# Optimization experiments

Hardware: AMD Instinct MI355X
Metric: run time of the kernel (lower is better)

## Reference

```python
import jax, jax.numpy as jnp
import numpy as np

NUM_HEADS = 4
IN_CHANNELS = 256
SCALE = IN_CHANNELS ** (-0.5)  # scaled=True uses in_channels, not hidden


def setup_inputs() -> dict:
    key = jax.random.key(0)
    ks = jax.random.split(key, 6)
    B, C, H, W = 8, 256, 48, 48
    hid = 128
    std_e = (2.0 / (3 * hid)) ** 0.5   # kaiming fan_out for 1x1 conv
    std_o = (2.0 / C) ** 0.5
    return {
        "x0": jax.random.normal(ks[0], (B, C, H, W), jnp.float32),
        "x1": jax.random.normal(ks[1], (B, C, H, W), jnp.float32),
        "embed_w0": jax.random.normal(ks[2], (3 * hid, C), jnp.float32) * std_e,
        "embed_b0": jnp.zeros((3 * hid,), jnp.float32),
        "embed_w1": jax.random.normal(ks[3], (3 * hid, C), jnp.float32) * std_e,
        "embed_b1": jnp.zeros((3 * hid,), jnp.float32),
        "out_w0": jax.random.normal(ks[4], (hid * NUM_HEADS, C), jnp.float32) * std_o,
        "out_b0": jnp.zeros((C,), jnp.float32),
        "out_w1": jax.random.normal(ks[5], (hid * NUM_HEADS, C), jnp.float32) * std_o,
        "out_b1": jnp.zeros((C,), jnp.float32),
    }


def _embed(x, w, b):
    # 1x1 conv: [B,C,H,W] x [3h,C] -> [B,3h,H,W], then flatten spatial and split q/k/v
    e = jnp.einsum('bchw,oc->bohw', x, w) + b[None, :, None, None]
    B, O, H, W = e.shape
    e = e.reshape(B, O, H * W)
    return jnp.split(e, 3, axis=1)  # each [B, h, N]


def _attend(q, k, v):
    # q from the OTHER stream; softmax over keys (last dim)
    attn = jax.nn.softmax(jnp.einsum('bcm,bcn->bmn', q, k) * SCALE, axis=-1)
    return jnp.einsum('bmn,bcn->bcm', attn, v)  # [B, h, N]


def _output(h, x, w, b):
    # all NUM_HEADS heads are identical (same embed conv reused per head),
    # so the concat along channels is a tile of one head.
    hh = jnp.tile(h, (1, NUM_HEADS, 1))  # [B, h*nh, N]
    # 1x1 transposed conv == pointwise linear with weight [h*nh, C]
    o = jnp.einsum('bcm,co->bom', hh, w) + b[None, :, None]
    return o.reshape(x.shape) + x  # residual


def reference(x0, x1, embed_w0, embed_b0, embed_w1, embed_b1,
              out_w0, out_b0, out_w1, out_b1):
    q0, k0, v0 = _embed(x0, embed_w0, embed_b0)
    q1, k1, v1 = _embed(x1, embed_w1, embed_b1)
    h0 = _attend(q1, k0, v0)  # stream 0 queried by stream 1's q
    h1 = _attend(q0, k1, v1)
    out0 = _output(h0, x0, out_w0, out_b0)
    out1 = _output(h1, x1, out_w1, out_b1)
    return (out0, out1)
```

## Files before the change

### kernel.cpp

```cpp
#include <hip/hip_runtime.h>
#include <stdint.h>

#define B_   8
#define C_   256
#define N_   2304
#define HID  128
#define O3   384
#define NH   4
#define SCALE 0.0625f
#define QPRE 0.09016844f

typedef unsigned short u16;
typedef short  bf8  __attribute__((ext_vector_type(8)));
typedef float  f4   __attribute__((ext_vector_type(4)));
typedef u16    u16x8 __attribute__((ext_vector_type(8)));
typedef u16    u16x4 __attribute__((ext_vector_type(4)));

#define MFMA(a,b,c) __builtin_amdgcn_mfma_f32_16x16x32_bf16((a),(b),(c),0,0,0)

static __device__ __forceinline__ u16 f2bf(float f){
    union { float f; unsigned int i; } v; v.f = f;
    unsigned int r = v.i + 0x7FFFu + ((v.i >> 16) & 1u);
    return (u16)(r >> 16);
}
static __device__ __forceinline__ float fexp2(float x){
#if __has_builtin(__builtin_amdgcn_exp2f)
    return __builtin_amdgcn_exp2f(x);
#else
    return __expf(x * 0.69314718f);
#endif
}
static __device__ __forceinline__ u16 hi16(float f){
    union { float f; unsigned int i; } v; v.f = f;
    return (u16)(v.i >> 16);
}
static __device__ __forceinline__ void dma16(const void* g, void* l){
    __builtin_amdgcn_global_load_lds(
        (const __attribute__((address_space(1))) void*)g,
        (__attribute__((address_space(3))) void*)l, 16, 0, 0);
}

__global__ __launch_bounds__(256, 4) void k_embed_fused(
        const float* __restrict__ x0, const float* __restrict__ x1,
        const float* __restrict__ ew0, const float* __restrict__ ew1,
        const float* __restrict__ ow0, const float* __restrict__ ow1,
        const float* __restrict__ b0, const float* __restrict__ b1,
        u16* __restrict__ Qc, u16* __restrict__ Kc, u16* __restrict__ Vc,
        u16* __restrict__ weff){
    __shared__ __align__(16) u16 tmp[256*36];
    __shared__ __align__(16) u16 Xs[32*280];
    int t = threadIdx.x;

    if (blockIdx.y == 16){
        int bx = blockIdx.x;
        if (bx >= 64) return;
        int gid = bx*256 + t;
        int s = gid >> 13, oc = (gid >> 5) & 255, hc0 = (gid & 31) * 4;
        const float* w = s ? ow1 : ow0;
        u16x4 v;
        #pragma unroll
        for (int i = 0; i < 4; ++i){
            float acc = 0.f;
            #pragma unroll
            for (int h = 0; h < NH; ++h) acc += w[(h*HID + hc0 + i)*C_ + oc];
            v[i] = f2bf(acc);
        }
        *reinterpret_cast<u16x4*>(&weff[(s*C_ + oc)*HID + hc0]) = v;
        return;
    }

    int z = blockIdx.y, bb = z >> 1, s = z & 1;
    const float* X    = (s ? x1 : x0) + (size_t)bb * (C_ * N_);
    const float* Wf32 = s ? ew1 : ew0;
    const float* bias = s ? b1 : b0;
    int n0 = blockIdx.x * 32;
    int lane = t & 63, wave = t >> 6;
    int l16 = lane & 15, quad = lane >> 4;

    {
        int cbase = t >> 3, cq = t & 7;
        float4 xr[8];
        #pragma unroll
        for (int rep = 0; rep < 8; ++rep)
            xr[rep] = *reinterpret_cast<const float4*>(
                &X[(size_t)(cbase + rep*32) * N_ + n0 + cq*4]);
        #pragma unroll
        for (int rep = 0; rep < 8; ++rep){
            int c = cbase + rep*32;
            u16x4 v;
            v[0] = f2bf(xr[rep].x); v[1] = f2bf(xr[rep].y);
            v[2] = f2bf(xr[rep].z); v[3] = f2bf(xr[rep].w);
            *reinterpret_cast<u16x4*>(&tmp[c*36 + cq*4]) = v;
        }
    }
    __syncthreads();
    {
        int n = t & 31, c8b = t >> 5;
        #pragma unroll
        for (int rep = 0; rep < 4; ++rep){
            int c8 = c8b + rep*8;
            u16x8 v;
            #pragma unroll
            for (int j = 0; j < 8; ++j) v[j] = tmp[(c8*8 + j)*36 + n];
            *reinterpret_cast<u16x8*>(&Xs[n*280 + c8*8]) = v;
        }
    }
    __syncthreads();

    size_t zq = (size_t)z * (N_ * HID);
    int ncw = blockIdx.x >> 1;
    u16* Es = tmp;
    for (int og = 0; og < 6; ++og){
        int o0 = og*64 + wave*16;
        f4 acc[2] = {f4{0,0,0,0}, f4{0,0,0,0}};
        #pragma unroll
        for (int kk = 0; kk < 8; ++kk){
            const float* wp = &Wf32[(size_t)(o0 + l16)*C_ + kk*32 + quad*8];
            float4 wa = *reinterpret_cast<const float4*>(wp);
            float4 wb = *reinterpret_cast<const float4*>(wp + 4);
            bf8 a;
            a[0] = (short)f2bf(wa.x); a[1] = (short)f2bf(wa.y);
            a[2] = (short)f2bf(wa.z); a[3] = (short)f2bf(wa.w);
            a[4] = (short)f2bf(wb.x); a[5] = (short)f2bf(wb.y);
            a[6] = (short)f2bf(wb.z); a[7] = (short)f2bf(wb.w);
            #pragma unroll
            for (int nt = 0; nt < 2; ++nt){
                bf8 bv = *reinterpret_cast<const bf8*>(
                    &Xs[(nt*16 + l16)*280 + kk*32 + quad*8]);
                acc[nt] = MFMA(a, bv, acc[nt]);
            }
        }
        float4 bv4 = *reinterpret_cast<const float4*>(&bias[o0 + quad*4]);
        float bb4[4] = {bv4.x, bv4.y, bv4.z, bv4.w};
        #pragma unroll
        for (int nt = 0; nt < 2; ++nt)
            #pragma unroll
            for (int r = 0; r < 4; ++r){
                float e = acc[nt][r] + bb4[r];
                if (og < 2) e *= QPRE;
                Es[(wave*16 + quad*4 + r)*40 + nt*16 + l16] = f2bf(e);
            }
        __syncthreads();
        if (og < 2){
            int n = t & 31, g8 = t >> 5;
            u16x8 v;
            #pragma unroll
            for (int j = 0; j < 8; ++j) v[j] = Es[(g8*8 + j)*40 + n];
            int ng = n0 + n;
            *reinterpret_cast<u16x8*>(&Qc[zq + (size_t)(ng>>4)*2048
                    + (og*8 + g8)*128 + (ng & 15)*8]) = v;
        } else if (og < 4){
            int n = t & 31, cc = t >> 5;
            u16x8 v;
            #pragma unroll
            for (int j = 0; j < 8; ++j) v[j] = Es[(cc*8 + j)*40 + n];
            *reinterpret_cast<u16x8*>(&Kc[zq + (size_t)(ncw*16 + (og-2)*8 + cc)*512
                    + ((n0 + n) & 63)*8]) = v;
        } else {
            int hl = t & 63, pp = t >> 6;
            u16x8 v = *reinterpret_cast<const u16x8*>(&Es[hl*40 + pp*8]);
            int p = ((n0 + pp*8) >> 3) & 7;
            *reinterpret_cast<u16x8*>(&Vc[zq + (size_t)(ncw*8 + p)*1024
                    + ((og-4)*64 + hl)*8]) = v;
        }
        __syncthreads();
    }
}

__global__ __launch_bounds__(256, 3) void k_attn_out(const u16* __restrict__ Qt,
        const u16* __restrict__ Kc, const u16* __restrict__ Vc,
        const u16* __restrict__ weff,
        const float* __restrict__ ob0, const float* __restrict__ ob1,
        const float* __restrict__ x0, const float* __restrict__ x1,
        float* __restrict__ out){
    __shared__ __align__(16) u16 kbuf[64*128];
    __shared__ __align__(16) u16 vbuf[64*128];
    __shared__ __align__(16) u16 smem[8*16*72];
    int bx = blockIdx.x;
    int xcd = bx & 7, t = bx >> 3;
    int z  = xcd*2 + (t >= 36 ? 1 : 0);
    int mt = (t >= 36) ? (t - 36) : t;
    int b = z >> 1, s = z & 1;
    const u16* Q = Qt + (size_t)(b*2 + (1 - s)) * (N_ * HID);
    const u16* K = Kc + (size_t)(b*2 + s)       * (N_ * HID);
    const u16* V = Vc + (size_t)(b*2 + s)       * (N_ * HID);
    const u16* Wf   = weff + (size_t)s * (C_ * HID);
    const float* bias = s ? ob1 : ob0;
    const float* X = (s ? x1 : x0) + (size_t)b * (C_ * N_);
    float* O = out + (size_t)s * ((size_t)B_ * C_ * N_) + (size_t)b * (C_ * N_);
    int lane = threadIdx.x & 63, wave = threadIdx.x >> 6;
    int l16 = lane & 15, quad = lane >> 4;
    int m0 = mt * 64 + wave * 16;

    bf8 aq[4];
    {
        const u16* Qb = Q + (size_t)(m0 >> 4)*2048 + l16*8;
        #pragma unroll
        for (int kk = 0; kk < 4; ++kk)
            aq[kk] = *reinterpret_cast<const bf8*>(&Qb[(kk*4 + quad)*128]);
    }

    bf8 ones;
    #pragma unroll
    for (int j = 0; j < 8; ++j) ones[j] = (short)0x3F80;

    f4 oacc[8];
    #pragma unroll
    for (int ct = 0; ct < 8; ++ct) oacc[ct] = f4{0,0,0,0};
    f4 sumacc = f4{0,0,0,0};

    const char* Kb = (const char*)K;
    const char* Vb = (const char*)V;

    for (int nc = 0; nc < N_/64; ++nc){
        __syncthreads();
        #pragma unroll
        for (int j = 0; j < 4; ++j){
            int ik = wave*4 + j;
            dma16(Kb + ((size_t)(nc*16 + ik)*512 + lane*8)*2, &kbuf[ik*512]);
        }
        #pragma unroll
        for (int j = 0; j < 4; ++j){
            int iv = wave*4 + j;
            dma16(Vb + ((size_t)(nc*8 + (iv>>1))*1024 + (iv&1)*512 + lane*8)*2,
                  &vbuf[iv*512]);
        }
        __syncthreads();
        f4 sacc[4] = {f4{0,0,0,0}, f4{0,0,0,0}, f4{0,0,0,0}, f4{0,0,0,0}};
        #pragma unroll
        for (int kk = 0; kk < 4; ++kk)
            #pragma unroll
            for (int nt = 0; nt < 4; ++nt){
                bf8 bk = *reinterpret_cast<const bf8*>(&kbuf[((kk*4+quad)*64 + nt*16 + l16)*8]);
                sacc[nt] = MFMA(aq[kk], bk, sacc[nt]);
            }
        u16* pw = smem + (wave*2 + (nc & 1)) * (16*72);
        #pragma unroll
        for (int nt = 0; nt < 4; ++nt)
            #pragma unroll
            for (int r = 0; r < 4; ++r)
                pw[(quad*4 + r)*72 + nt*16 + l16] = hi16(fexp2(sacc[nt][r]));
        #pragma unroll
        for (int kk2 = 0; kk2 < 2; ++kk2){
            bf8 ap = *reinterpret_cast<const bf8*>(&pw[l16*72 + kk2*32 + quad*8]);
            sumacc = MFMA(ap, ones, sumacc);
            #pragma unroll
            for (int ct = 0; ct < 8; ++ct){
                bf8 bv = *reinterpret_cast<const bf8*>(&vbuf[((kk2*4+quad)*128 + ct*16 + l16)*8]);
                oacc[ct] = MFMA(ap, bv, oacc[ct]);
            }
        }
    }

    __syncthreads();
    float inv[4];
    #pragma unroll
    for (int r = 0; r < 4; ++r) inv[r] = 1.0f / sumacc[r];
    #pragma unroll
    for (int ct = 0; ct < 8; ++ct)
        #pragma unroll
        for (int r = 0; r < 4; ++r)
            smem[(wave*16 + quad*4 + r)*136 + ct*16 + l16] = f2bf(oacc[ct][r] * inv[r]);
    __syncthreads();

    int mb = mt * 64;
    int oc0 = wave * 64;
    f4 acc2[4][4];
    #pragma unroll
    for (int ot = 0; ot < 4; ++ot)
        #pragma unroll
        for (int nt = 0; nt < 4; ++nt) acc2[ot][nt] = f4{0,0,0,0};
    #pragma unroll
    for (int kk = 0; kk < 4; ++kk){
        bf8 bh[4];
        #pragma unroll
        for (int nt = 0; nt < 4; ++nt)
            bh[nt] = *reinterpret_cast<const bf8*>(&smem[(nt*16 + l16)*136 + kk*32 + quad*8]);
        #pragma unroll
        for (int ot = 0; ot < 4; ++ot){
            bf8 a = *reinterpret_cast<const bf8*>(&Wf[(oc0 + ot*16 + l16)*HID + kk*32 + quad*8]);
            #pragma unroll
            for (int nt = 0; nt < 4; ++nt)
                acc2[ot][nt] = MFMA(a, bh[nt], acc2[ot][nt]);
        }
    }
    #pragma unroll
    for (int ot = 0; ot < 4; ++ot)
        #pragma unroll
        for (int nt = 0; nt < 4; ++nt){
            int m = mb + nt*16 + l16;
            #pragma unroll
            for (int r = 0; r < 4; ++r){
                int oc = oc0 + ot*16 + quad*4 + r;
                O[(size_t)oc*N_ + m] = acc2[ot][nt][r] + bias[oc] + X[(size_t)oc*N_ + m];
            }
        }
}

extern "C" void kernel_launch(void* const* d_in, const int* in_sizes, int n_in,
                              void* d_out, int out_size, void* d_ws, size_t ws_size,
                              hipStream_t stream){
    const float* x0  = (const float*)d_in[0];
    const float* x1  = (const float*)d_in[1];
    const float* ew0 = (const float*)d_in[2];
    const float* eb0 = (const float*)d_in[3];
    const float* ew1 = (const float*)d_in[4];
    const float* eb1 = (const float*)d_in[5];
    const float* ow0 = (const float*)d_in[6];
    const float* ob0 = (const float*)d_in[7];
    const float* ow1 = (const float*)d_in[8];
    const float* ob1 = (const float*)d_in[9];

    u16* ws = (u16*)d_ws;
    const size_t QT_E = (size_t)16 * N_ * HID;
    u16* Qc   = ws;
    u16* Kc   = Qc + QT_E;
    u16* Vc   = Kc + QT_E;
    u16* weff = Vc + QT_E;

    k_embed_fused<<<dim3(72, 17), dim3(256), 0, stream>>>(
        x0, x1, ew0, ew1, ow0, ow1, eb0, eb1, Qc, Kc, Vc, weff);
    k_attn_out   <<<dim3(576),    dim3(256), 0, stream>>>(
        Qc, Kc, Vc, weff, ob0, ob1, x0, x1, (float*)d_out);
}
```

Measured before the change: 243.6 us.

## Pre-convert embed weights to bf16 in a prep kernel and double-buffer the epilogue

Adds a separate prep kernel that converts the embedding weights to bf16 once and computes the summed output weights. The embed kernel now loads bf16 A fragments directly instead of loading and converting fp32 weights in every block, and drops the extra weff grid row. The epilogue staging buffer alternates between two halves so one __syncthreads per output group can be removed. The cost is an extra kernel launch and a serial dependency before the embed kernel.

```diff
diff --git a/kernel.cpp b/kernel.cpp
--- a/kernel.cpp
+++ b/kernel.cpp
@@ -40,40 +40,46 @@
         (__attribute__((address_space(3))) void*)l, 16, 0, 0);
 }
 
+__global__ __launch_bounds__(256) void k_prep(const float* __restrict__ ew0,
+                                              const float* __restrict__ ew1,
+                                              const float* __restrict__ ow0,
+                                              const float* __restrict__ ow1,
+                                              u16* __restrict__ Wbf,
+                                              u16* __restrict__ weff){
+    int bid = blockIdx.x;
+    if (bid < 192){
+        int s = bid >= 96 ? 1 : 0;
+        int xb = bid - s*96;
+        const float* w = s ? ew1 : ew0;
+        u16* o = Wbf + (size_t)s * (O3 * C_);
+        int idx = (xb * 256 + threadIdx.x) * 4;
+        float4 v = *reinterpret_cast<const float4*>(&w[idx]);
+        o[idx+0] = f2bf(v.x); o[idx+1] = f2bf(v.y);
+        o[idx+2] = f2bf(v.z); o[idx+3] = f2bf(v.w);
+    } else {
+        int gid = (bid - 192) * 256 + threadIdx.x;
+        int oc = gid & 255, hc = (gid >> 8) & 127, s = gid >> 15;
+        const float* w = s ? ow1 : ow0;
+        float acc = 0.f;
+        #pragma unroll
+        for (int h = 0; h < NH; ++h) acc += w[(h*HID + hc)*C_ + oc];
+        weff[(s*C_ + oc)*HID + hc] = f2bf(acc);
+    }
+}
+
 __global__ __launch_bounds__(256, 4) void k_embed_fused(
         const float* __restrict__ x0, const float* __restrict__ x1,
-        const float* __restrict__ ew0, const float* __restrict__ ew1,
-        const float* __restrict__ ow0, const float* __restrict__ ow1,
+        const u16* __restrict__ Wbf,
         const float* __restrict__ b0, const float* __restrict__ b1,
-        u16* __restrict__ Qc, u16* __restrict__ Kc, u16* __restrict__ Vc,
-        u16* __restrict__ weff){
+        u16* __restrict__ Qc, u16* __restrict__ Kc, u16* __restrict__ Vc){
     __shared__ __align__(16) u16 tmp[256*36];
     __shared__ __align__(16) u16 Xs[32*280];
-    int t = threadIdx.x;
-
-    if (blockIdx.y == 16){
-        int bx = blockIdx.x;
-        if (bx >= 64) return;
-        int gid = bx*256 + t;
-        int s = gid >> 13, oc = (gid >> 5) & 255, hc0 = (gid & 31) * 4;
-        const float* w = s ? ow1 : ow0;
-        u16x4 v;
-        #pragma unroll
-        for (int i = 0; i < 4; ++i){
-            float acc = 0.f;
-            #pragma unroll
-            for (int h = 0; h < NH; ++h) acc += w[(h*HID + hc0 + i)*C_ + oc];
-            v[i] = f2bf(acc);
-        }
-        *reinterpret_cast<u16x4*>(&weff[(s*C_ + oc)*HID + hc0]) = v;
-        return;
-    }
-
     int z = blockIdx.y, bb = z >> 1, s = z & 1;
-    const float* X    = (s ? x1 : x0) + (size_t)bb * (C_ * N_);
-    const float* Wf32 = s ? ew1 : ew0;
+    const float* X = (s ? x1 : x0) + (size_t)bb * (C_ * N_);
+    const u16* W = Wbf + (size_t)s * (O3 * C_);
     const float* bias = s ? b1 : b0;
     int n0 = blockIdx.x * 32;
+    int t = threadIdx.x;
     int lane = t & 63, wave = t >> 6;
     int l16 = lane & 15, quad = lane >> 4;
 
@@ -109,20 +115,13 @@
 
     size_t zq = (size_t)z * (N_ * HID);
     int ncw = blockIdx.x >> 1;
-    u16* Es = tmp;
     for (int og = 0; og < 6; ++og){
+        u16* Es = tmp + (og & 1) * 2560;
         int o0 = og*64 + wave*16;
         f4 acc[2] = {f4{0,0,0,0}, f4{0,0,0,0}};
         #pragma unroll
         for (int kk = 0; kk < 8; ++kk){
-            const float* wp = &Wf32[(size_t)(o0 + l16)*C_ + kk*32 + quad*8];
-            float4 wa = *reinterpret_cast<const float4*>(wp);
-            float4 wb = *reinterpret_cast<const float4*>(wp + 4);
-            bf8 a;
-            a[0] = (short)f2bf(wa.x); a[1] = (short)f2bf(wa.y);
-            a[2] = (short)f2bf(wa.z); a[3] = (short)f2bf(wa.w);
-            a[4] = (short)f2bf(wb.x); a[5] = (short)f2bf(wb.y);
-            a[6] = (short)f2bf(wb.z); a[7] = (short)f2bf(wb.w);
+            bf8 a = *reinterpret_cast<const bf8*>(&W[(o0 + l16)*C_ + kk*32 + quad*8]);
             #pragma unroll
             for (int nt = 0; nt < 2; ++nt){
                 bf8 bv = *reinterpret_cast<const bf8*>(
@@ -163,7 +162,6 @@
             *reinterpret_cast<u16x8*>(&Vc[zq + (size_t)(ncw*8 + p)*1024
                     + ((og-4)*64 + hl)*8]) = v;
         }
-        __syncthreads();
     }
 }
 
@@ -316,10 +314,11 @@
     u16* Qc   = ws;
     u16* Kc   = Qc + QT_E;
     u16* Vc   = Kc + QT_E;
-    u16* weff = Vc + QT_E;
-
-    k_embed_fused<<<dim3(72, 17), dim3(256), 0, stream>>>(
-        x0, x1, ew0, ew1, ow0, ow1, eb0, eb1, Qc, Kc, Vc, weff);
-    k_attn_out   <<<dim3(576),    dim3(256), 0, stream>>>(
-        Qc, Kc, Vc, weff, ob0, ob1, x0, x1, (float*)d_out);
-}
+    u16* Wbf  = Vc + QT_E;
+    u16* weff = Wbf + (size_t)2 * O3 * C_;
+
+    k_prep       <<<dim3(448),    dim3(256), 0, stream>>>(ew0, ew1, ow0, ow1, Wbf, weff);
+    k_embed_fused<<<dim3(72, 16), dim3(256), 0, stream>>>(x0, x1, Wbf, eb0, eb1, Qc, Kc, Vc);
+    k_attn_out   <<<dim3(576),    dim3(256), 0, stream>>>(Qc, Kc, Vc, weff, ob0, ob1,
+                                                          x0, x1, (float*)d_out);
+}
```

Result: faster. 222.1 us (-8.8%).
